# Kernel tuning notes

Measured on AMD Instinct MI355X. Metric: run time of the kernel, lower is better.

Reference implementation:

```python
import jax, jax.numpy as jnp
import numpy as np
import math

C = 256
N_HEAD = 8
GROUPS = 16
EPS = 1e-5


def group_norm(x, w, b):
    # x: [B, C, H, W]; biased variance over (group_channels, H, W), like torch GroupNorm
    B, Cc, H, W = x.shape
    xg = x.reshape(B, GROUPS, Cc // GROUPS, H, W)
    mean = xg.mean(axis=(2, 3, 4), keepdims=True)
    var = ((xg - mean) ** 2).mean(axis=(2, 3, 4), keepdims=True)
    xn = ((xg - mean) * jax.lax.rsqrt(var + EPS)).reshape(B, Cc, H, W)
    return xn * w[None, :, None, None] + b[None, :, None, None]


def setup_inputs() -> dict:
    key = jax.random.key(0)
    k0, k1, k2, k3, k4, k5 = jax.random.split(key, 6)
    B, H, W = 4, 48, 48
    input_feat = jax.random.normal(k0, (B, C, H, W), dtype=jnp.float32)
    gn_weight = jnp.ones((C,), dtype=jnp.float32) + 0.02 * jax.random.normal(k1, (C,), dtype=jnp.float32)
    gn_bias = 0.02 * jax.random.normal(k2, (C,), dtype=jnp.float32)
    w_qkv = jax.random.normal(k3, (3 * C, C), dtype=jnp.float32) / math.sqrt(C)  # Conv2d 1x1, no bias
    w_out = jax.random.normal(k4, (C, C), dtype=jnp.float32) / math.sqrt(C)      # Conv2d 1x1
    b_out = 0.02 * jax.random.normal(k5, (C,), dtype=jnp.float32)
    return {"input_feat": input_feat, "gn_weight": gn_weight, "gn_bias": gn_bias,
            "w_qkv": w_qkv, "w_out": w_out, "b_out": b_out}


def reference(input_feat, gn_weight, gn_bias, w_qkv, w_out, b_out):
    # H=W=48 <= max_attn_size=48 -> full attention branch
    B, Cc, H, W = input_feat.shape
    n, d = N_HEAD, Cc // N_HEAD
    S = H * W
    normed = group_norm(input_feat, gn_weight, gn_bias)
    # 1x1 conv QKV: [B, 3C, H, W]
    qkv = jnp.einsum('oc,bchw->bohw', w_qkv, normed)
    # view(B, n, 3*d, H, W).chunk(3, dim=2) == reshape to (B, n, 3, d, S)
    qkv = qkv.reshape(B, n, 3, d, S)
    q, k, v = qkv[:, :, 0], qkv[:, :, 1], qkv[:, :, 2]  # each [B, n, d, S]
    # NOTE: original divides by sqrt(channel), not sqrt(head_dim)
    scale = 1.0 / math.sqrt(Cc)
    scores = jnp.einsum('bnds,bndt->bnst', q, k) * scale  # [B, n, S, S]
    attn = jax.nn.softmax(scores, axis=-1)
    o = jnp.einsum('bnst,bndt->bnds', attn, v)  # [B, n, d, S]
    o = o.reshape(B, Cc, H, W)
    out = jnp.einsum('oc,bchw->bohw', w_out, o) + b_out[None, :, None, None]
    return out + input_feat
```

## Files before the change

### kernel.cpp

```cpp
#include <hip/hip_runtime.h>
#include <hip/hip_bf16.h>
#include <stdint.h>

#define S    2304
#define CHN  256
#define BATCH 4
#define QS   0.09016844005556021f

typedef __attribute__((ext_vector_type(8))) short bf16x8;
typedef __attribute__((ext_vector_type(4))) float f32x4;
typedef __attribute__((ext_vector_type(2))) uint32_t u32x2;
typedef __attribute__((ext_vector_type(4))) unsigned short u16x4;
typedef unsigned short u16;

#define AS1 __attribute__((address_space(1)))
#define AS3 __attribute__((address_space(3)))
#define GLDS(gptr, lptr) __builtin_amdgcn_global_load_lds((const AS1 void*)(gptr), (AS3 void*)(lptr), 16, 0, 0)

__device__ __forceinline__ u16 f2bf(float f) {
  union { float f; uint32_t u; } v; v.f = f;
  uint32_t u = v.u;
  u += 0x7fffu + ((u >> 16) & 1u);
  return (u16)(u >> 16);
}
__device__ __forceinline__ float bf2f(u16 h) {
  union { uint32_t u; float f; } v; v.u = ((uint32_t)h) << 16;
  return v.f;
}
__device__ __forceinline__ uint32_t pk_bf16(float a, float b) {
  union { __hip_bfloat162 h; uint32_t u; } cv;
  cv.h = __float22bfloat162_rn(make_float2(a, b));
  return cv.u;
}

__global__ void k_prep(const float* __restrict__ wq, const float* __restrict__ wo,
                       u16* __restrict__ wq_bf, u16* __restrict__ wo_bf) {
  int i = blockIdx.x * 256 + threadIdx.x;
  if (i < 768 * 256) wq_bf[i] = f2bf(wq[i]);
  int j = i - 768 * 256;
  if (j >= 0 && j < 256 * 256) wo_bf[j] = f2bf(wo[j]);
}

__global__ void k_gnstats(const float* __restrict__ x, float2* __restrict__ stats) {
  int bg = blockIdx.x;
  const float4* p = (const float4*)(x + (size_t)bg * 36864);
  float s = 0.f, ss = 0.f;
  for (int i = threadIdx.x; i < 9216; i += 1024) {
    float4 v = p[i];
    s  += v.x + v.y + v.z + v.w;
    ss += v.x * v.x + v.y * v.y + v.z * v.z + v.w * v.w;
  }
  int lane = threadIdx.x & 63, wv = threadIdx.x >> 6;
  for (int m = 1; m < 64; m <<= 1) { s += __shfl_xor(s, m, 64); ss += __shfl_xor(ss, m, 64); }
  __shared__ float rs[16], rss[16];
  if (lane == 0) { rs[wv] = s; rss[wv] = ss; }
  __syncthreads();
  if (threadIdx.x == 0) {
    float S_ = 0.f, SS = 0.f;
    for (int i = 0; i < 16; ++i) { S_ += rs[i]; SS += rss[i]; }
    float mean = S_ / 36864.f;
    float var  = SS / 36864.f - mean * mean;
    stats[bg] = make_float2(mean, rsqrtf(var + 1e-5f));
  }
}

__global__ void k_gnnorm(const float* __restrict__ x, const float* __restrict__ w,
                         const float* __restrict__ bias, const float2* __restrict__ stats,
                         u16* __restrict__ nt) {
  int bid = blockIdx.x;
  int b = bid / 144, r = bid % 144;
  int sblk = r >> 2, cq = r & 3;
  int t = threadIdx.x;
  int ni = t & 63, cgrp = t >> 6;
  int s = sblk * 64 + ni;
  int cbase = cq * 64 + cgrp * 16;
  float2 stg = stats[b * 16 + (cbase >> 4)];
  bf16x8 v0, v1;
  #pragma unroll
  for (int e = 0; e < 16; ++e) {
    int c = cbase + e;
    float val = x[(size_t)(b * 256 + c) * S + s];
    float xn = (val - stg.x) * stg.y * w[c] + bias[c];
    if (e < 8) v0[e] = (short)f2bf(xn); else v1[e - 8] = (short)f2bf(xn);
  }
  u16* dst = nt + (size_t)(b * S + s) * 256 + cbase;
  *(bf16x8*)dst = v0;
  *(bf16x8*)(dst + 8) = v1;
}

__global__ __launch_bounds__(256) void k_qkv(const u16* __restrict__ A,
                                             const u16* __restrict__ Bm,
                                             u16* __restrict__ qkt,
                                             u16* __restrict__ vt) {
  __shared__ __align__(16) u16 As[2][64 * 32];
  __shared__ __align__(16) u16 Bs[2][128 * 32];
  int tid = threadIdx.x, lane = tid & 63, w = tid >> 6;
  int wr = w >> 1, wc = w & 1;
  int cb = lane & 15, q4 = lane >> 4;
  int m0 = blockIdx.y * 64, n0 = blockIdx.x * 128;

  const u16* gA0 = A  + (size_t)(m0 + (tid >> 2)) * 256 + (tid & 3) * 8;
  const u16* gB0 = Bm + (size_t)(n0 + (tid >> 2)) * 256 + (tid & 3) * 8;
  const u16* gB1 = gB0 + 64 * 256;
  char* lA = (char*)&As[0][0] + (w << 10);
  char* lB = (char*)&Bs[0][0] + (w << 10);

  #define STAGE_Q(buf, k0) do {                      \
    GLDS(gA0 + (k0), lA + (buf) * 4096);             \
    GLDS(gB0 + (k0), lB + (buf) * 8192);             \
    GLDS(gB1 + (k0), lB + (buf) * 8192 + 4096);      \
  } while (0)

  f32x4 zero4 = {0.f, 0.f, 0.f, 0.f};
  f32x4 acc[2][4];
  for (int i = 0; i < 2; ++i) for (int j = 0; j < 4; ++j) acc[i][j] = zero4;

  STAGE_Q(0, 0);
  __syncthreads();
  for (int ks = 0; ks < 8; ++ks) {
    int cur = ks & 1;
    if (ks < 7) STAGE_Q(cur ^ 1, (ks + 1) * 32);
    const u16* as = &As[cur][0];
    const u16* bs = &Bs[cur][0];
    bf16x8 af[2], bfr[4];
    for (int i = 0; i < 2; ++i)
      af[i]  = *(const bf16x8*)&as[(wr * 32 + i * 16 + cb) * 32 + 8 * q4];
    for (int j = 0; j < 4; ++j)
      bfr[j] = *(const bf16x8*)&bs[(wc * 64 + j * 16 + cb) * 32 + 8 * q4];
    for (int i = 0; i < 2; ++i)
      for (int j = 0; j < 4; ++j)
        acc[i][j] = __builtin_amdgcn_mfma_f32_16x16x32_bf16(af[i], bfr[j], acc[i][j], 0, 0, 0);
    __syncthreads();
  }

  for (int i = 0; i < 2; ++i)
    for (int j = 0; j < 4; ++j) {
      int ob = m0 + wr * 32 + i * 16 + q4 * 4;
      int n  = n0 + wc * 64 + j * 16 + cb;
      int h = ob / 96, oq = ob % 96;
      if (oq < 64) {
        float sc = (oq < 32) ? QS : 1.f;
        u16x4 pk;
        for (int r = 0; r < 4; ++r) pk[r] = f2bf(acc[i][j][r] * sc);
        *(u16x4*)&qkt[(size_t)n * 512 + h * 64 + oq] = pk;
      } else {
        for (int r = 0; r < 4; ++r)
          vt[(size_t)(h * 32 + oq - 64 + r) * 9216 + n] = f2bf(acc[i][j][r]);
      }
    }
  #undef STAGE_Q
}

__global__ __launch_bounds__(256) void k_attn(const u16* __restrict__ qkt,
                                              const u16* __restrict__ vt,
                                              u16* __restrict__ ot) {
  __shared__ __align__(16) u16 Ks[2][64 * 32];
  __shared__ __align__(16) u16 Vd[2][32 * 64];
  __shared__ __align__(16) u16 Ps[4][16 * 64];

  int tid = threadIdx.x, lane = tid & 63, w = tid >> 6;
  int cb = lane & 15, g4 = lane >> 4;
  int hw = blockIdx.x;
  int orig = (hw & 7) * 144 + (hw >> 3);
  int bh = orig / 36, bx = orig % 36;
  int b = bh >> 3, h = bh & 7;
  int q0 = bx * 64 + w * 16;

  const u16* kbase = qkt + (size_t)(b * S) * 512 + h * 64 + 32;
  const u16* vbase = vt + (size_t)(h * 32) * 9216 + (size_t)b * S;
  u16* Pw = &Ps[w][0];

  bf16x8 qf = *(const bf16x8*)&qkt[(size_t)(b * S + q0 + cb) * 512 + h * 64 + 8 * g4];

  f32x4 zero4 = {0.f, 0.f, 0.f, 0.f};
  f32x4 acc_o[2]; acc_o[0] = zero4; acc_o[1] = zero4;
  float l = 0.f;

  int xk = (cb ^ (cb >> 2)) & 3;
  int sw7 = cb & 7;

  int krow = tid >> 2, kch = (tid & 3) ^ ((krow ^ (krow >> 2)) & 3);
  int vrow = tid >> 3, vch = (tid & 7) ^ (vrow & 7);
  const u16* gK0 = kbase + (size_t)krow * 512 + kch * 8;
  const u16* gV0 = vbase + (size_t)vrow * 9216 + vch * 8;
  char* ldsK = (char*)&Ks[0][0] + (w << 10);
  char* ldsV = (char*)&Vd[0][0] + (w << 10);

  #define STAGE_A(buf, t0) do {                                   \
    GLDS(gK0 + (size_t)(t0) * 512, ldsK + (buf) * 4096);           \
    GLDS(gV0 + (t0),               ldsV + (buf) * 4096);           \
  } while (0)

  STAGE_A(0, 0);
  __syncthreads();

  for (int t0 = 0; t0 < S; t0 += 64) {
    int cur = (t0 >> 6) & 1;
    if (t0 + 64 < S) STAGE_A(cur ^ 1, t0 + 64);
    const u16* KsC = &Ks[cur][0];
    const u16* VdC = &Vd[cur][0];

    bf16x8 kf[4];
    for (int k4 = 0; k4 < 4; ++k4)
      kf[k4] = *(const bf16x8*)&KsC[(16 * k4 + cb) * 32 + ((g4 ^ xk) * 8)];

    f32x4 pacc[4];
    __builtin_amdgcn_s_setprio(1);
    for (int k4 = 0; k4 < 4; ++k4)
      pacc[k4] = __builtin_amdgcn_mfma_f32_16x16x32_bf16(kf[k4], qf, zero4, 0, 0, 0);
    __builtin_amdgcn_s_setprio(0);

    float lacc = 0.f;
    for (int k4 = 0; k4 < 4; ++k4) {
      f32x4 p = pacc[k4];
      float e0 = __builtin_amdgcn_exp2f(p[0]);
      float e1 = __builtin_amdgcn_exp2f(p[1]);
      float e2 = __builtin_amdgcn_exp2f(p[2]);
      float e3 = __builtin_amdgcn_exp2f(p[3]);
      lacc += (e0 + e1) + (e2 + e3);
      u32x2 pk = { pk_bf16(e0, e1), pk_bf16(e2, e3) };
      int idx = cb * 64 + (((2 * k4 + (g4 >> 1)) ^ sw7) << 3) + ((g4 & 1) << 2);
      *(u32x2*)&Pw[idx] = pk;
    }
    l += lacc;
    asm volatile("s_waitcnt lgkmcnt(0)" ::: "memory");

    __builtin_amdgcn_s_setprio(1);
    bf16x8 pa[2];
    for (int kk = 0; kk < 2; ++kk)
      pa[kk] = *(const bf16x8*)&Pw[cb * 64 + (((4 * kk + g4) ^ sw7) << 3)];
    for (int jd = 0; jd < 2; ++jd)
      for (int kk = 0; kk < 2; ++kk) {
        bf16x8 vb = *(const bf16x8*)&VdC[(16 * jd + cb) * 64 + (((4 * kk + g4) ^ sw7) << 3)];
        acc_o[jd] = __builtin_amdgcn_mfma_f32_16x16x32_bf16(pa[kk], vb, acc_o[jd], 0, 0, 0);
      }
    __builtin_amdgcn_s_setprio(0);

    __syncthreads();
  }

  float v = l;
  v += __shfl_xor(v, 16, 64);
  v += __shfl_xor(v, 32, 64);
  float linv = __builtin_amdgcn_rcpf(v);
  for (int r = 0; r < 4; ++r) {
    float li = __shfl(linv, 4 * g4 + r, 64);
    int sq = q0 + 4 * g4 + r;
    for (int jd = 0; jd < 2; ++jd) {
      int c = h * 32 + 16 * jd + cb;
      ot[(size_t)(b * S + sq) * 256 + c] = f2bf(acc_o[jd][r] * li);
    }
  }
  #undef STAGE_A
}

__global__ __launch_bounds__(256) void k_oproj(const u16* __restrict__ A,
                                               const u16* __restrict__ Bm,
                                               float* __restrict__ out,
                                               const float* __restrict__ bias,
                                               const float* __restrict__ resid) {
  __shared__ __align__(16) u16 As[2][64 * 32];
  __shared__ __align__(16) u16 Bs[2][64 * 32];
  int tid = threadIdx.x, lane = tid & 63, w = tid >> 6;
  int cb = lane & 15, q4 = lane >> 4;
  int m0 = blockIdx.y * 64, n0 = blockIdx.x * 64;

  const u16* gA0 = A  + (size_t)(m0 + (tid >> 2)) * 256 + (tid & 3) * 8;
  const u16* gB0 = Bm + (size_t)(n0 + (tid >> 2)) * 256 + (tid & 3) * 8;
  char* lA = (char*)&As[0][0] + (w << 10);
  char* lB = (char*)&Bs[0][0] + (w << 10);

  #define STAGE_O(buf, k0) do {                      \
    GLDS(gA0 + (k0), lA + (buf) * 4096);             \
    GLDS(gB0 + (k0), lB + (buf) * 4096);             \
  } while (0)

  f32x4 zero4 = {0.f, 0.f, 0.f, 0.f};
  f32x4 acc[4];
  for (int j = 0; j < 4; ++j) acc[j] = zero4;

  STAGE_O(0, 0);
  __syncthreads();
  for (int ks = 0; ks < 8; ++ks) {
    int cur = ks & 1;
    if (ks < 7) STAGE_O(cur ^ 1, (ks + 1) * 32);
    const u16* as = &As[cur][0];
    const u16* bs = &Bs[cur][0];
    bf16x8 af = *(const bf16x8*)&as[(w * 16 + cb) * 32 + 8 * q4];
    bf16x8 bfr[4];
    for (int j = 0; j < 4; ++j)
      bfr[j] = *(const bf16x8*)&bs[(j * 16 + cb) * 32 + 8 * q4];
    for (int j = 0; j < 4; ++j)
      acc[j] = __builtin_amdgcn_mfma_f32_16x16x32_bf16(af, bfr[j], acc[j], 0, 0, 0);
    __syncthreads();
  }

  for (int j = 0; j < 4; ++j)
    for (int r = 0; r < 4; ++r) {
      int o = m0 + w * 16 + q4 * 4 + r;
      int n = n0 + j * 16 + cb;
      int b = n / S, s2 = n % S;
      size_t gi = (size_t)(b * 256 + o) * S + s2;
      out[gi] = acc[j][r] + bias[o] + resid[gi];
    }
  #undef STAGE_O
}

extern "C" void kernel_launch(void* const* d_in, const int* in_sizes, int n_in,
                              void* d_out, int out_size, void* d_ws, size_t ws_size,
                              hipStream_t stream) {
  const float* input = (const float*)d_in[0];
  const float* gnw   = (const float*)d_in[1];
  const float* gnb   = (const float*)d_in[2];
  const float* wqkv  = (const float*)d_in[3];
  const float* wout  = (const float*)d_in[4];
  const float* bout  = (const float*)d_in[5];
  float* out = (float*)d_out;
  char* ws = (char*)d_ws;

  size_t o_wq  = 0;
  size_t o_wo  = o_wq + (size_t)768 * 256 * 2;
  size_t o_st  = o_wo + (size_t)256 * 256 * 2;
  size_t o_nt  = o_st + 1024;
  size_t o_qkt = o_nt + (size_t)9216 * 256 * 2;
  size_t o_vt  = o_qkt + (size_t)9216 * 512 * 2;
  size_t o_ot  = o_vt + (size_t)256 * 9216 * 2;

  u16*    wq_bf = (u16*)(ws + o_wq);
  u16*    wo_bf = (u16*)(ws + o_wo);
  float2* stats = (float2*)(ws + o_st);
  u16*    nt    = (u16*)(ws + o_nt);
  u16*    qkt   = (u16*)(ws + o_qkt);
  u16*    vt    = (u16*)(ws + o_vt);
  u16*    otb   = (u16*)(ws + o_ot);

  k_prep<<<1024, 256, 0, stream>>>(wqkv, wout, wq_bf, wo_bf);
  k_gnstats<<<64, 1024, 0, stream>>>(input, stats);
  k_gnnorm<<<576, 256, 0, stream>>>(input, gnw, gnb, stats, nt);
  k_qkv<<<dim3(72, 12), 256, 0, stream>>>(wq_bf, nt, qkt, vt);
  k_attn<<<1152, 256, 0, stream>>>(qkt, vt, otb);
  k_oproj<<<dim3(144, 4), 256, 0, stream>>>(wo_bf, otb, out, bout, input);
}
```

Measured before the change: 94.39 us.

## Split attention over two key halves and combine partial outputs in a new kernel

The attention kernel now splits each query tile's 2304 keys into two halves processed by separate blocks, doubling the grid to 2304 blocks. Each block writes unnormalized bf16 partial outputs and row sums, and a new k_comb kernel adds the two halves and normalizes them. The key loop is also unrolled by two with precomputed LDS pointers and a scheduling barrier. This adds parallelism and cuts the per-block loop length, at the cost of an extra launch, extra global traffic for the partials, and an added bf16 rounding of each partial before the sum.

```diff
diff --git a/kernel.cpp b/kernel.cpp
--- a/kernel.cpp
+++ b/kernel.cpp
@@ -5,6 +5,7 @@
 #define S    2304
 #define CHN  256
 #define BATCH 4
+#define NKEYS 1152
 #define QS   0.09016844005556021f
 
 typedef __attribute__((ext_vector_type(8))) short bf16x8;
@@ -153,7 +154,8 @@
 
 __global__ __launch_bounds__(256) void k_attn(const u16* __restrict__ qkt,
                                               const u16* __restrict__ vt,
-                                              u16* __restrict__ ot) {
+                                              u16* __restrict__ otP,
+                                              float* __restrict__ lsum) {
   __shared__ __align__(16) u16 Ks[2][64 * 32];
   __shared__ __align__(16) u16 Vd[2][32 * 64];
   __shared__ __align__(16) u16 Ps[4][16 * 64];
@@ -161,14 +163,14 @@
   int tid = threadIdx.x, lane = tid & 63, w = tid >> 6;
   int cb = lane & 15, g4 = lane >> 4;
   int hw = blockIdx.x;
-  int orig = (hw & 7) * 144 + (hw >> 3);
-  int bh = orig / 36, bx = orig % 36;
+  int orig = (hw & 7) * 288 + (hw >> 3);
+  int bh = orig / 72, rem = orig % 72;
+  int qtile = rem >> 1, split = rem & 1;
   int b = bh >> 3, h = bh & 7;
-  int q0 = bx * 64 + w * 16;
-
-  const u16* kbase = qkt + (size_t)(b * S) * 512 + h * 64 + 32;
-  const u16* vbase = vt + (size_t)(h * 32) * 9216 + (size_t)b * S;
-  u16* Pw = &Ps[w][0];
+  int q0 = qtile * 64 + w * 16;
+
+  const u16* kbase = qkt + (size_t)(b * S) * 512 + h * 64 + 32 + (size_t)split * NKEYS * 512;
+  const u16* vbase = vt + (size_t)(h * 32) * 9216 + (size_t)b * S + split * NKEYS;
 
   bf16x8 qf = *(const bf16x8*)&qkt[(size_t)(b * S + q0 + cb) * 512 + h * 64 + 8 * g4];
 
@@ -179,79 +181,122 @@
   int xk = (cb ^ (cb >> 2)) & 3;
   int sw7 = cb & 7;
 
+  const u16* p_kf[4];
+  #pragma unroll
+  for (int k4 = 0; k4 < 4; ++k4)
+    p_kf[k4] = &Ks[0][(16 * k4 + cb) * 32 + ((g4 ^ xk) * 8)];
+  u16* p_pw[4];
+  #pragma unroll
+  for (int k4 = 0; k4 < 4; ++k4)
+    p_pw[k4] = &Ps[w][cb * 64 + (((2 * k4 + (g4 >> 1)) ^ sw7) << 3) + ((g4 & 1) << 2)];
+  const u16* p_pa[2];
+  #pragma unroll
+  for (int kk = 0; kk < 2; ++kk)
+    p_pa[kk] = &Ps[w][cb * 64 + (((4 * kk + g4) ^ sw7) << 3)];
+  const u16* p_vb[2][2];
+  #pragma unroll
+  for (int jd = 0; jd < 2; ++jd)
+    #pragma unroll
+    for (int kk = 0; kk < 2; ++kk)
+      p_vb[jd][kk] = &Vd[0][(16 * jd + cb) * 64 + (((4 * kk + g4) ^ sw7) << 3)];
+
   int krow = tid >> 2, kch = (tid & 3) ^ ((krow ^ (krow >> 2)) & 3);
   int vrow = tid >> 3, vch = (tid & 7) ^ (vrow & 7);
-  const u16* gK0 = kbase + (size_t)krow * 512 + kch * 8;
-  const u16* gV0 = vbase + (size_t)vrow * 9216 + vch * 8;
+  const u16* gK = kbase + (size_t)krow * 512 + kch * 8;
+  const u16* gV = vbase + (size_t)vrow * 9216 + vch * 8;
   char* ldsK = (char*)&Ks[0][0] + (w << 10);
   char* ldsV = (char*)&Vd[0][0] + (w << 10);
 
-  #define STAGE_A(buf, t0) do {                                   \
-    GLDS(gK0 + (size_t)(t0) * 512, ldsK + (buf) * 4096);           \
-    GLDS(gV0 + (t0),               ldsV + (buf) * 4096);           \
+  #define STAGE_A(buf) do {                          \
+    GLDS(gK, ldsK + (buf) * 4096);                   \
+    GLDS(gV, ldsV + (buf) * 4096);                   \
+    gK += 64 * 512; gV += 64;                        \
   } while (0)
 
-  STAGE_A(0, 0);
+  #define TILE(buf, pf) do {                                                   \
+    if (pf) STAGE_A(buf ^ 1);                                                  \
+    bf16x8 kf[4];                                                              \
+    _Pragma("unroll")                                                          \
+    for (int k4 = 0; k4 < 4; ++k4)                                             \
+      kf[k4] = *(const bf16x8*)(p_kf[k4] + (buf) * 2048);                      \
+    f32x4 pacc[4];                                                             \
+    __builtin_amdgcn_s_setprio(1);                                             \
+    _Pragma("unroll")                                                          \
+    for (int k4 = 0; k4 < 4; ++k4)                                             \
+      pacc[k4] = __builtin_amdgcn_mfma_f32_16x16x32_bf16(kf[k4], qf, zero4, 0, 0, 0); \
+    __builtin_amdgcn_s_setprio(0);                                             \
+    float lacc = 0.f;                                                          \
+    _Pragma("unroll")                                                          \
+    for (int k4 = 0; k4 < 4; ++k4) {                                           \
+      f32x4 p = pacc[k4];                                                      \
+      float e0 = __builtin_amdgcn_exp2f(p[0]);                                 \
+      float e1 = __builtin_amdgcn_exp2f(p[1]);                                 \
+      float e2 = __builtin_amdgcn_exp2f(p[2]);                                 \
+      float e3 = __builtin_amdgcn_exp2f(p[3]);                                 \
+      lacc += (e0 + e1) + (e2 + e3);                                           \
+      u32x2 pk = { pk_bf16(e0, e1), pk_bf16(e2, e3) };                         \
+      *(u32x2*)p_pw[k4] = pk;                                                  \
+    }                                                                          \
+    l += lacc;                                                                 \
+    asm volatile("s_waitcnt lgkmcnt(0)" ::: "memory");                         \
+    __builtin_amdgcn_sched_barrier(0);                                         \
+    __builtin_amdgcn_s_setprio(1);                                             \
+    bf16x8 pa[2];                                                              \
+    _Pragma("unroll")                                                          \
+    for (int kk = 0; kk < 2; ++kk)                                             \
+      pa[kk] = *(const bf16x8*)p_pa[kk];                                       \
+    _Pragma("unroll")                                                          \
+    for (int jd = 0; jd < 2; ++jd)                                             \
+      _Pragma("unroll")                                                        \
+      for (int kk = 0; kk < 2; ++kk) {                                         \
+        bf16x8 vb = *(const bf16x8*)(p_vb[jd][kk] + (buf) * 2048);             \
+        acc_o[jd] = __builtin_amdgcn_mfma_f32_16x16x32_bf16(pa[kk], vb, acc_o[jd], 0, 0, 0); \
+      }                                                                        \
+    __builtin_amdgcn_s_setprio(0);                                             \
+    __syncthreads();                                                           \
+  } while (0)
+
+  STAGE_A(0);
   __syncthreads();
-
-  for (int t0 = 0; t0 < S; t0 += 64) {
-    int cur = (t0 >> 6) & 1;
-    if (t0 + 64 < S) STAGE_A(cur ^ 1, t0 + 64);
-    const u16* KsC = &Ks[cur][0];
-    const u16* VdC = &Vd[cur][0];
-
-    bf16x8 kf[4];
-    for (int k4 = 0; k4 < 4; ++k4)
-      kf[k4] = *(const bf16x8*)&KsC[(16 * k4 + cb) * 32 + ((g4 ^ xk) * 8)];
-
-    f32x4 pacc[4];
-    __builtin_amdgcn_s_setprio(1);
-    for (int k4 = 0; k4 < 4; ++k4)
-      pacc[k4] = __builtin_amdgcn_mfma_f32_16x16x32_bf16(kf[k4], qf, zero4, 0, 0, 0);
-    __builtin_amdgcn_s_setprio(0);
-
-    float lacc = 0.f;
-    for (int k4 = 0; k4 < 4; ++k4) {
-      f32x4 p = pacc[k4];
-      float e0 = __builtin_amdgcn_exp2f(p[0]);
-      float e1 = __builtin_amdgcn_exp2f(p[1]);
-      float e2 = __builtin_amdgcn_exp2f(p[2]);
-      float e3 = __builtin_amdgcn_exp2f(p[3]);
-      lacc += (e0 + e1) + (e2 + e3);
-      u32x2 pk = { pk_bf16(e0, e1), pk_bf16(e2, e3) };
-      int idx = cb * 64 + (((2 * k4 + (g4 >> 1)) ^ sw7) << 3) + ((g4 & 1) << 2);
-      *(u32x2*)&Pw[idx] = pk;
-    }
-    l += lacc;
-    asm volatile("s_waitcnt lgkmcnt(0)" ::: "memory");
-
-    __builtin_amdgcn_s_setprio(1);
-    bf16x8 pa[2];
-    for (int kk = 0; kk < 2; ++kk)
-      pa[kk] = *(const bf16x8*)&Pw[cb * 64 + (((4 * kk + g4) ^ sw7) << 3)];
-    for (int jd = 0; jd < 2; ++jd)
-      for (int kk = 0; kk < 2; ++kk) {
-        bf16x8 vb = *(const bf16x8*)&VdC[(16 * jd + cb) * 64 + (((4 * kk + g4) ^ sw7) << 3)];
-        acc_o[jd] = __builtin_amdgcn_mfma_f32_16x16x32_bf16(pa[kk], vb, acc_o[jd], 0, 0, 0);
-      }
-    __builtin_amdgcn_s_setprio(0);
-
-    __syncthreads();
+  for (int it = 0; it < 9; ++it) {
+    TILE(0, 1);
+    TILE(1, it < 8);
   }
 
   float v = l;
   v += __shfl_xor(v, 16, 64);
   v += __shfl_xor(v, 32, 64);
-  float linv = __builtin_amdgcn_rcpf(v);
+  if (lane < 16)
+    lsum[(size_t)(bh * 2 + split) * S + q0 + lane] = v;
+
+  u16* op = otP + (size_t)split * 9216 * 256;
   for (int r = 0; r < 4; ++r) {
-    float li = __shfl(linv, 4 * g4 + r, 64);
     int sq = q0 + 4 * g4 + r;
     for (int jd = 0; jd < 2; ++jd) {
       int c = h * 32 + 16 * jd + cb;
-      ot[(size_t)(b * S + sq) * 256 + c] = f2bf(acc_o[jd][r] * li);
+      op[(size_t)(b * S + sq) * 256 + c] = f2bf(acc_o[jd][r]);
     }
   }
   #undef STAGE_A
+  #undef TILE
+}
+
+__global__ void k_comb(const u16* __restrict__ otP, const float* __restrict__ lsum,
+                       u16* __restrict__ ot) {
+  int gid = blockIdx.x * 256 + threadIdx.x;
+  int n = gid >> 5, c8 = gid & 31;
+  int b = n / S, s = n - b * S;
+  int h = c8 >> 2;
+  float l0 = lsum[(size_t)((b * 8 + h) * 2 + 0) * S + s];
+  float l1 = lsum[(size_t)((b * 8 + h) * 2 + 1) * S + s];
+  float inv = __builtin_amdgcn_rcpf(l0 + l1);
+  bf16x8 a = *(const bf16x8*)&otP[(size_t)n * 256 + c8 * 8];
+  bf16x8 bb = *(const bf16x8*)&otP[(size_t)9216 * 256 + (size_t)n * 256 + c8 * 8];
+  bf16x8 o;
+  #pragma unroll
+  for (int e = 0; e < 8; ++e)
+    o[e] = (short)f2bf((bf2f((u16)a[e]) + bf2f((u16)bb[e])) * inv);
+  *(bf16x8*)&ot[(size_t)n * 256 + c8 * 8] = o;
 }
 
 __global__ __launch_bounds__(256) void k_oproj(const u16* __restrict__ A,
@@ -324,7 +369,8 @@
   size_t o_nt  = o_st + 1024;
   size_t o_qkt = o_nt + (size_t)9216 * 256 * 2;
   size_t o_vt  = o_qkt + (size_t)9216 * 512 * 2;
-  size_t o_ot  = o_vt + (size_t)256 * 9216 * 2;
+  size_t o_oP  = o_vt + (size_t)256 * 9216 * 2;
+  size_t o_ls  = o_oP + (size_t)2 * 9216 * 256 * 2;
 
   u16*    wq_bf = (u16*)(ws + o_wq);
   u16*    wo_bf = (u16*)(ws + o_wo);
@@ -332,12 +378,15 @@
   u16*    nt    = (u16*)(ws + o_nt);
   u16*    qkt   = (u16*)(ws + o_qkt);
   u16*    vt    = (u16*)(ws + o_vt);
-  u16*    otb   = (u16*)(ws + o_ot);
+  u16*    otP   = (u16*)(ws + o_oP);
+  float*  lsum  = (float*)(ws + o_ls);
+  u16*    otb   = (u16*)(ws + o_nt);
 
   k_prep<<<1024, 256, 0, stream>>>(wqkv, wout, wq_bf, wo_bf);
   k_gnstats<<<64, 1024, 0, stream>>>(input, stats);
   k_gnnorm<<<576, 256, 0, stream>>>(input, gnw, gnb, stats, nt);
   k_qkv<<<dim3(72, 12), 256, 0, stream>>>(wq_bf, nt, qkt, vt);
-  k_attn<<<1152, 256, 0, stream>>>(qkt, vt, otb);
+  k_attn<<<2304, 256, 0, stream>>>(qkt, vt, otP, lsum);
+  k_comb<<<1152, 256, 0, stream>>>(otP, lsum, otb);
   k_oproj<<<dim3(144, 4), 256, 0, stream>>>(wo_bf, otb, out, bout, input);
 }
```

Measured after the change: 93.21 us. No clear change (-1.2%).
